# Performance work log

Measured on AMD Instinct MI355X. Metric: run time of the kernel, lower is better.

## Reference

```python
import jax, jax.numpy as jnp
import numpy as np

H = 64  # LSTM units for both layers
T = 128  # sequence length
D = 128  # input feature dim
B = 2048  # batch

def setup_inputs() -> dict:
    key = jax.random.key(0)
    ks = jax.random.split(key, 7)
    s_in = 1.0 / np.sqrt(D)
    s_h = 1.0 / np.sqrt(H)
    return {
        "x": jax.random.normal(ks[0], (B, T, D), dtype=jnp.float32),
        # Keras LSTM weights: kernel [in, 4H], recurrent_kernel [H, 4H], bias [4H]
        # gate order: i, f, g (cell candidate), o
        "W1": jax.random.normal(ks[1], (D, 4 * H), dtype=jnp.float32) * s_in,
        "U1": jax.random.normal(ks[2], (H, 4 * H), dtype=jnp.float32) * s_h,
        "b1": jnp.zeros((4 * H,), dtype=jnp.float32),
        "W2": jax.random.normal(ks[3], (H, 4 * H), dtype=jnp.float32) * s_h,
        "U2": jax.random.normal(ks[4], (H, 4 * H), dtype=jnp.float32) * s_h,
        "b2": jnp.zeros((4 * H,), dtype=jnp.float32),
    }

def _lstm(x, W, U, b, act):
    """Keras-faithful LSTM, return_sequences=True, zero init state.
    x: [B, T, D_in] -> hs: [B, T, H]
    recurrent_activation = sigmoid; `act` is the cell/output activation.
    """
    Bsz = x.shape[0]
    # Precompute input projections for all timesteps (one big GEMM).
    xz = jnp.einsum('btd,dg->btg', x, W) + b  # [B, T, 4H]
    xz = jnp.swapaxes(xz, 0, 1)  # [T, B, 4H]

    def step(carry, zt):
        h, c = carry
        z = zt + h @ U  # [B, 4H]
        i, f, g, o = jnp.split(z, 4, axis=-1)
        i = jax.nn.sigmoid(i)
        f = jax.nn.sigmoid(f)
        g = act(g)
        o = jax.nn.sigmoid(o)
        c = f * c + i * g
        h = o * act(c)
        return (h, c), h

    init = (jnp.zeros((Bsz, H), x.dtype), jnp.zeros((Bsz, H), x.dtype))
    _, hs = jax.lax.scan(step, init, xz)  # hs: [T, B, H]
    return jnp.swapaxes(hs, 0, 1)  # [B, T, H]

def reference(x, W1, U1, b1, W2, U2, b2):
    h1 = _lstm(x, W1, U1, b1, jnp.tanh)           # layer 1: default tanh
    h2 = _lstm(h1, W2, U2, b2, jax.nn.sigmoid)    # layer 2: activation='sigmoid'
    return h2.reshape(h2.shape[0], T * H, 1)      # Reshape((8192, 1))
```

## Files before the change

### kernel.cpp

```cpp
#include <hip/hip_runtime.h>
#include <stdint.h>

typedef __attribute__((ext_vector_type(8))) short short8;
typedef __attribute__((ext_vector_type(2))) short short2_t;
typedef __attribute__((ext_vector_type(4))) float floatx4;

#define TT 128
#define DD 128

#define BARRIER_LDS() asm volatile("s_waitcnt lgkmcnt(0)\n\ts_barrier" ::: "memory")

__device__ __forceinline__ short f2bf(float f) {
  union { float f; uint32_t u; } v; v.f = f;
  uint32_t u = v.u;
  u += 0x7fffu + ((u >> 16) & 1u);
  return (short)(u >> 16);
}

__device__ __forceinline__ float sigf(float x) {
  return __builtin_amdgcn_rcpf(1.f + __expf(-x));
}
__device__ __forceinline__ float tanhf_(float x) {
  return 2.f * __builtin_amdgcn_rcpf(1.f + __expf(-2.f * x)) - 1.f;
}

__global__ void wtrans_all(const float* __restrict__ W1, const float* __restrict__ U1,
                           const float* __restrict__ W2, const float* __restrict__ U2,
                           short* __restrict__ w1t, short* __restrict__ u1t,
                           short* __restrict__ w2t, short* __restrict__ u2t) {
  int n = blockIdx.x;
  int k = threadIdx.x;
  w1t[n * 128 + k] = f2bf(W1[k * 256 + n]);
  if (k < 64) {
    u1t[n * 64 + k] = f2bf(U1[k * 256 + n]);
    w2t[n * 64 + k] = f2bf(W2[k * 256 + n]);
    u2t[n * 64 + k] = f2bf(U2[k * 256 + n]);
  }
}

__global__ __launch_bounds__(256, 2) void lstm_fused(
    const float* __restrict__ x,
    const short* __restrict__ w1t, const short* __restrict__ u1t,
    const short* __restrict__ w2t, const short* __restrict__ u2t,
    const float* __restrict__ b1, const float* __restrict__ b2,
    float* __restrict__ out) {
  __shared__ short hb1[2][4 * 80];
  __shared__ short hb2[2][4 * 80];
  __shared__ short xbuf[2][4 * 144];

  const int tid = threadIdx.x;
  const int w = tid >> 6;
  const int lane = tid & 63;
  const int mrow = lane & 15;
  const int quad = lane >> 4;
  const int rowbase = blockIdx.x * 4;
  const int colw = w * 16 + mrow;
  const int br_a = mrow >> 2;

  short8 w1r[4][4], u1r[4][2], w2r[4][2], u2r[4][2];
#pragma unroll
  for (int g = 0; g < 4; ++g) {
    const int n = g * 4 + w;
#pragma unroll
    for (int s = 0; s < 4; ++s)
      w1r[g][s] = *(const short8*)(w1t + n * 2048 + mrow * 128 + quad * 8 + s * 32);
#pragma unroll
    for (int s = 0; s < 2; ++s) {
      u1r[g][s] = *(const short8*)(u1t + n * 1024 + mrow * 64 + quad * 8 + s * 32);
      w2r[g][s] = *(const short8*)(w2t + n * 1024 + mrow * 64 + quad * 8 + s * 32);
      u2r[g][s] = *(const short8*)(u2t + n * 1024 + mrow * 64 + quad * 8 + s * 32);
    }
  }
  float bias1[4], bias2[4];
#pragma unroll
  for (int g = 0; g < 4; ++g) {
    bias1[g] = b1[g * 64 + colw];
    bias2[g] = b2[g * 64 + colw];
  }

  const int xr = tid >> 6;
  const int xc = (tid & 63) * 2;
  const float* xload = x + (size_t)(rowbase + xr) * (TT * DD) + xc;

  {
    short* z = (short*)hb2;
    for (int i = tid; i < 2 * 4 * 80; i += 256) z[i] = 0;
    float a0 = xload[0], a1 = xload[1];
    *(short2_t*)&xbuf[1][xr * 144 + xc] = short2_t{f2bf(a0), f2bf(a1)};
  }
  BARRIER_LDS();
  short8 xf[4];
#pragma unroll
  for (int s = 0; s < 4; ++s)
    xf[s] = *(const short8*)&xbuf[1][br_a * 144 + (quad + 4 * s) * 8];
  float xr0 = xload[DD], xr1 = xload[DD + 1];

  short8 h1f[2], h2f[2];
#pragma unroll
  for (int s = 0; s < 2; ++s)
#pragma unroll
    for (int j = 0; j < 8; ++j) { h1f[s][j] = 0; h2f[s][j] = 0; }
  float c1 = 0.f, c2 = 0.f;

#pragma unroll 1
  for (int t = 0; t < TT; ++t) {
    const int p = t & 1;

    floatx4 acc[4];
#pragma unroll
    for (int g = 0; g < 4; ++g) acc[g] = floatx4{0.f, 0.f, 0.f, 0.f};
#pragma unroll
    for (int g = 0; g < 4; ++g) {
#pragma unroll
      for (int s = 0; s < 4; ++s)
        acc[g] = __builtin_amdgcn_mfma_f32_16x16x32_bf16(xf[s], w1r[g][s], acc[g], 0, 0, 0);
#pragma unroll
      for (int s = 0; s < 2; ++s)
        acc[g] = __builtin_amdgcn_mfma_f32_16x16x32_bf16(h1f[s], u1r[g][s], acc[g], 0, 0, 0);
    }

    *(short2_t*)&xbuf[p][xr * 144 + xc] = short2_t{f2bf(xr0), f2bf(xr1)};
    {
      int tn = (t + 2 < TT) ? t + 2 : TT - 1;
      xr0 = xload[(size_t)tn * DD];
      xr1 = xload[(size_t)tn * DD + 1];
    }

    {
      float ig = sigf(acc[0][0] + bias1[0]);
      float fg = sigf(acc[1][0] + bias1[1]);
      float gg = tanhf_(acc[2][0] + bias1[2]);
      float og = sigf(acc[3][0] + bias1[3]);
      float c = fg * c1 + ig * gg;
      c1 = c;
      float h = og * tanhf_(c);
      hb1[p][quad * 80 + colw] = f2bf(h);
    }

    BARRIER_LDS();

#pragma unroll
    for (int s = 0; s < 2; ++s) {
      h1f[s] = *(const short8*)&hb1[p][br_a * 80 + (quad + 4 * s) * 8];
      h2f[s] = *(const short8*)&hb2[1 - p][br_a * 80 + (quad + 4 * s) * 8];
    }
#pragma unroll
    for (int s = 0; s < 4; ++s)
      xf[s] = *(const short8*)&xbuf[p][br_a * 144 + (quad + 4 * s) * 8];

    floatx4 bcc[4];
#pragma unroll
    for (int g = 0; g < 4; ++g) bcc[g] = floatx4{0.f, 0.f, 0.f, 0.f};
#pragma unroll
    for (int g = 0; g < 4; ++g) {
#pragma unroll
      for (int s = 0; s < 2; ++s)
        bcc[g] = __builtin_amdgcn_mfma_f32_16x16x32_bf16(h1f[s], w2r[g][s], bcc[g], 0, 0, 0);
#pragma unroll
      for (int s = 0; s < 2; ++s)
        bcc[g] = __builtin_amdgcn_mfma_f32_16x16x32_bf16(h2f[s], u2r[g][s], bcc[g], 0, 0, 0);
    }

    {
      float ig = sigf(bcc[0][0] + bias2[0]);
      float fg = sigf(bcc[1][0] + bias2[1]);
      float gg = sigf(bcc[2][0] + bias2[2]);
      float og = sigf(bcc[3][0] + bias2[3]);
      float c = fg * c2 + ig * gg;
      c2 = c;
      float h = og * sigf(c);
      hb2[p][quad * 80 + colw] = f2bf(h);
      out[(size_t)(rowbase + quad) * 8192 + t * 64 + colw] = h;
    }
  }
}

extern "C" void kernel_launch(void* const* d_in, const int* in_sizes, int n_in,
                              void* d_out, int out_size, void* d_ws, size_t ws_size,
                              hipStream_t stream) {
  const float* x  = (const float*)d_in[0];
  const float* W1 = (const float*)d_in[1];
  const float* U1 = (const float*)d_in[2];
  const float* b1 = (const float*)d_in[3];
  const float* W2 = (const float*)d_in[4];
  const float* U2 = (const float*)d_in[5];
  const float* b2 = (const float*)d_in[6];
  float* out = (float*)d_out;

  short* w1t = (short*)d_ws;
  short* u1t = w1t + 32768;
  short* w2t = u1t + 16384;
  short* u2t = w2t + 16384;

  hipLaunchKernelGGL(wtrans_all, dim3(256), dim3(128), 0, stream,
                     W1, U1, W2, U2, w1t, u1t, w2t, u2t);
  hipLaunchKernelGGL(lstm_fused, dim3(512), dim3(256), 0, stream,
                     x, w1t, u1t, w2t, u2t, b1, b2, out);
}
```

Baseline: 316.7 us.

## Split LSTM layers across warp groups and pipeline layer 2 one step behind

Each block now processes 8 batch rows with 512 threads. Warps 0-3 run layer 1 while warps 4-7 run layer 2 one timestep behind, so the two layers execute concurrently with one barrier per step instead of running serially within the same warps. Each MFMA output tile now uses two of its four accumulator rows, which halves wasted MFMA work, and weights are split between the warp groups, lowering per-thread register pressure. The cost is an extra pipeline step, halved grid size (256 blocks), and layer-2 warps also taking over the x prefetch.

```diff
diff --git a/kernel.cpp b/kernel.cpp
--- a/kernel.cpp
+++ b/kernel.cpp
@@ -2,7 +2,7 @@
 #include <stdint.h>
 
 typedef __attribute__((ext_vector_type(8))) short short8;
-typedef __attribute__((ext_vector_type(2))) short short2_t;
+typedef __attribute__((ext_vector_type(4))) short short4_t;
 typedef __attribute__((ext_vector_type(4))) float floatx4;
 
 #define TT 128
@@ -38,139 +38,173 @@
   }
 }
 
-__global__ __launch_bounds__(256, 2) void lstm_fused(
+__global__ __launch_bounds__(512, 2) void lstm_fused(
     const float* __restrict__ x,
     const short* __restrict__ w1t, const short* __restrict__ u1t,
     const short* __restrict__ w2t, const short* __restrict__ u2t,
     const float* __restrict__ b1, const float* __restrict__ b2,
     float* __restrict__ out) {
-  __shared__ short hb1[2][4 * 80];
-  __shared__ short hb2[2][4 * 80];
-  __shared__ short xbuf[2][4 * 144];
+  __shared__ short hb1[2][8 * 80];
+  __shared__ short hb2[2][8 * 80];
+  __shared__ short xbuf[2][8 * 144];
 
   const int tid = threadIdx.x;
   const int w = tid >> 6;
+  const bool isL1 = (w < 4);
+  const int wg = w & 3;
   const int lane = tid & 63;
   const int mrow = lane & 15;
   const int quad = lane >> 4;
-  const int rowbase = blockIdx.x * 4;
-  const int colw = w * 16 + mrow;
-  const int br_a = mrow >> 2;
-
-  short8 w1r[4][4], u1r[4][2], w2r[4][2], u2r[4][2];
-#pragma unroll
-  for (int g = 0; g < 4; ++g) {
-    const int n = g * 4 + w;
+  const int rowbase = blockIdx.x * 8;
+  const int colw = wg * 16 + mrow;
+  const int br_a = 2 * (mrow >> 2) + (mrow & 1);
+
+  short8 wA[4][4], uA[4][2];
+  float bias[4];
+  if (isL1) {
+#pragma unroll
+    for (int g = 0; g < 4; ++g) {
+      const int n = g * 4 + wg;
+#pragma unroll
+      for (int s = 0; s < 4; ++s)
+        wA[g][s] = *(const short8*)(w1t + n * 2048 + mrow * 128 + quad * 8 + s * 32);
+#pragma unroll
+      for (int s = 0; s < 2; ++s)
+        uA[g][s] = *(const short8*)(u1t + n * 1024 + mrow * 64 + quad * 8 + s * 32);
+      bias[g] = b1[g * 64 + colw];
+    }
+  } else {
+#pragma unroll
+    for (int g = 0; g < 4; ++g) {
+      const int n = g * 4 + wg;
+#pragma unroll
+      for (int s = 0; s < 2; ++s) {
+        wA[g][s]     = *(const short8*)(w2t + n * 1024 + mrow * 64 + quad * 8 + s * 32);
+        wA[g][2 + s] = *(const short8*)(u2t + n * 1024 + mrow * 64 + quad * 8 + s * 32);
+      }
+      bias[g] = b2[g * 64 + colw];
+    }
+  }
+
+  const int tid2 = tid & 255;
+  const int sxr = tid2 >> 5;
+  const int sxc = (tid2 & 31) * 4;
+  const float* xload = x + (size_t)(rowbase + sxr) * (TT * DD) + sxc;
+
+  short8 h1f[2], xh[4];
+#pragma unroll
+  for (int s = 0; s < 2; ++s)
+#pragma unroll
+    for (int j = 0; j < 8; ++j) h1f[s][j] = 0;
+#pragma unroll
+  for (int s = 0; s < 4; ++s)
+#pragma unroll
+    for (int j = 0; j < 8; ++j) xh[s][j] = 0;
+  float cc[2] = {0.f, 0.f};
+  floatx4 xnext;
+
+  for (int idx = tid; idx < 2 * 8 * 80; idx += 512) ((short*)hb2)[idx] = 0;
+  if (!isL1) {
+    floatx4 x0 = *(const floatx4*)xload;
+    short4_t v;
+#pragma unroll
+    for (int j = 0; j < 4; ++j) v[j] = f2bf(x0[j]);
+    *(short4_t*)&xbuf[0][sxr * 144 + sxc] = v;
+    xnext = *(const floatx4*)(xload + DD);
+  }
+  BARRIER_LDS();
+  if (isL1) {
 #pragma unroll
     for (int s = 0; s < 4; ++s)
-      w1r[g][s] = *(const short8*)(w1t + n * 2048 + mrow * 128 + quad * 8 + s * 32);
-#pragma unroll
-    for (int s = 0; s < 2; ++s) {
-      u1r[g][s] = *(const short8*)(u1t + n * 1024 + mrow * 64 + quad * 8 + s * 32);
-      w2r[g][s] = *(const short8*)(w2t + n * 1024 + mrow * 64 + quad * 8 + s * 32);
-      u2r[g][s] = *(const short8*)(u2t + n * 1024 + mrow * 64 + quad * 8 + s * 32);
-    }
-  }
-  float bias1[4], bias2[4];
-#pragma unroll
-  for (int g = 0; g < 4; ++g) {
-    bias1[g] = b1[g * 64 + colw];
-    bias2[g] = b2[g * 64 + colw];
-  }
-
-  const int xr = tid >> 6;
-  const int xc = (tid & 63) * 2;
-  const float* xload = x + (size_t)(rowbase + xr) * (TT * DD) + xc;
-
-  {
-    short* z = (short*)hb2;
-    for (int i = tid; i < 2 * 4 * 80; i += 256) z[i] = 0;
-    float a0 = xload[0], a1 = xload[1];
-    *(short2_t*)&xbuf[1][xr * 144 + xc] = short2_t{f2bf(a0), f2bf(a1)};
-  }
-  BARRIER_LDS();
-  short8 xf[4];
-#pragma unroll
-  for (int s = 0; s < 4; ++s)
-    xf[s] = *(const short8*)&xbuf[1][br_a * 144 + (quad + 4 * s) * 8];
-  float xr0 = xload[DD], xr1 = xload[DD + 1];
-
-  short8 h1f[2], h2f[2];
-#pragma unroll
-  for (int s = 0; s < 2; ++s)
-#pragma unroll
-    for (int j = 0; j < 8; ++j) { h1f[s][j] = 0; h2f[s][j] = 0; }
-  float c1 = 0.f, c2 = 0.f;
+      xh[s] = *(const short8*)&xbuf[0][br_a * 144 + (quad + 4 * s) * 8];
+  }
+
+  float* outp = out + (size_t)rowbase * 8192 + colw;
 
 #pragma unroll 1
-  for (int t = 0; t < TT; ++t) {
-    const int p = t & 1;
-
-    floatx4 acc[4];
-#pragma unroll
-    for (int g = 0; g < 4; ++g) acc[g] = floatx4{0.f, 0.f, 0.f, 0.f};
-#pragma unroll
-    for (int g = 0; g < 4; ++g) {
-#pragma unroll
-      for (int s = 0; s < 4; ++s)
-        acc[g] = __builtin_amdgcn_mfma_f32_16x16x32_bf16(xf[s], w1r[g][s], acc[g], 0, 0, 0);
-#pragma unroll
-      for (int s = 0; s < 2; ++s)
-        acc[g] = __builtin_amdgcn_mfma_f32_16x16x32_bf16(h1f[s], u1r[g][s], acc[g], 0, 0, 0);
-    }
-
-    *(short2_t*)&xbuf[p][xr * 144 + xc] = short2_t{f2bf(xr0), f2bf(xr1)};
-    {
-      int tn = (t + 2 < TT) ? t + 2 : TT - 1;
-      xr0 = xload[(size_t)tn * DD];
-      xr1 = xload[(size_t)tn * DD + 1];
-    }
-
-    {
-      float ig = sigf(acc[0][0] + bias1[0]);
-      float fg = sigf(acc[1][0] + bias1[1]);
-      float gg = tanhf_(acc[2][0] + bias1[2]);
-      float og = sigf(acc[3][0] + bias1[3]);
-      float c = fg * c1 + ig * gg;
-      c1 = c;
-      float h = og * tanhf_(c);
-      hb1[p][quad * 80 + colw] = f2bf(h);
+  for (int i = 0; i <= TT; ++i) {
+    const int p = i & 1;
+
+    if (isL1) {
+      if (i < TT) {
+        floatx4 acc[4];
+#pragma unroll
+        for (int g = 0; g < 4; ++g) acc[g] = floatx4{0.f, 0.f, 0.f, 0.f};
+#pragma unroll
+        for (int g = 0; g < 4; ++g) {
+#pragma unroll
+          for (int s = 0; s < 4; ++s)
+            acc[g] = __builtin_amdgcn_mfma_f32_16x16x32_bf16(xh[s], wA[g][s], acc[g], 0, 0, 0);
+#pragma unroll
+          for (int s = 0; s < 2; ++s)
+            acc[g] = __builtin_amdgcn_mfma_f32_16x16x32_bf16(h1f[s], uA[g][s], acc[g], 0, 0, 0);
+        }
+#pragma unroll
+        for (int r = 0; r < 2; ++r) {
+          float ig = sigf(acc[0][r] + bias[0]);
+          float fg = sigf(acc[1][r] + bias[1]);
+          float gg = tanhf_(acc[2][r] + bias[2]);
+          float og = sigf(acc[3][r] + bias[3]);
+          float c = fg * cc[r] + ig * gg;
+          cc[r] = c;
+          float h = og * tanhf_(c);
+          hb1[p][(2 * quad + r) * 80 + colw] = f2bf(h);
+        }
+      }
+    } else {
+      {
+        short4_t v;
+#pragma unroll
+        for (int j = 0; j < 4; ++j) v[j] = f2bf(xnext[j]);
+        *(short4_t*)&xbuf[1 - p][sxr * 144 + sxc] = v;
+        int tn = (i + 2 < TT) ? i + 2 : TT - 1;
+        xnext = *(const floatx4*)(xload + (size_t)tn * DD);
+      }
+      if (i >= 1) {
+        floatx4 acc[4];
+#pragma unroll
+        for (int g = 0; g < 4; ++g) acc[g] = floatx4{0.f, 0.f, 0.f, 0.f};
+#pragma unroll
+        for (int g = 0; g < 4; ++g) {
+#pragma unroll
+          for (int s = 0; s < 2; ++s)
+            acc[g] = __builtin_amdgcn_mfma_f32_16x16x32_bf16(h1f[s], wA[g][s], acc[g], 0, 0, 0);
+#pragma unroll
+          for (int s = 0; s < 2; ++s)
+            acc[g] = __builtin_amdgcn_mfma_f32_16x16x32_bf16(xh[s], wA[g][2 + s], acc[g], 0, 0, 0);
+        }
+#pragma unroll
+        for (int r = 0; r < 2; ++r) {
+          float ig = sigf(acc[0][r] + bias[0]);
+          float fg = sigf(acc[1][r] + bias[1]);
+          float gg = sigf(acc[2][r] + bias[2]);
+          float og = sigf(acc[3][r] + bias[3]);
+          float c = fg * cc[r] + ig * gg;
+          cc[r] = c;
+          float h = og * sigf(c);
+          hb2[p][(2 * quad + r) * 80 + colw] = f2bf(h);
+          outp[(size_t)(2 * quad + r) * 8192 + (i - 1) * 64] = h;
+        }
+      }
     }
 
     BARRIER_LDS();
 
-#pragma unroll
-    for (int s = 0; s < 2; ++s) {
-      h1f[s] = *(const short8*)&hb1[p][br_a * 80 + (quad + 4 * s) * 8];
-      h2f[s] = *(const short8*)&hb2[1 - p][br_a * 80 + (quad + 4 * s) * 8];
-    }
-#pragma unroll
-    for (int s = 0; s < 4; ++s)
-      xf[s] = *(const short8*)&xbuf[p][br_a * 144 + (quad + 4 * s) * 8];
-
-    floatx4 bcc[4];
-#pragma unroll
-    for (int g = 0; g < 4; ++g) bcc[g] = floatx4{0.f, 0.f, 0.f, 0.f};
-#pragma unroll
-    for (int g = 0; g < 4; ++g) {
-#pragma unroll
-      for (int s = 0; s < 2; ++s)
-        bcc[g] = __builtin_amdgcn_mfma_f32_16x16x32_bf16(h1f[s], w2r[g][s], bcc[g], 0, 0, 0);
-#pragma unroll
-      for (int s = 0; s < 2; ++s)
-        bcc[g] = __builtin_amdgcn_mfma_f32_16x16x32_bf16(h2f[s], u2r[g][s], bcc[g], 0, 0, 0);
-    }
-
-    {
-      float ig = sigf(bcc[0][0] + bias2[0]);
-      float fg = sigf(bcc[1][0] + bias2[1]);
-      float gg = sigf(bcc[2][0] + bias2[2]);
-      float og = sigf(bcc[3][0] + bias2[3]);
-      float c = fg * c2 + ig * gg;
-      c2 = c;
-      float h = og * sigf(c);
-      hb2[p][quad * 80 + colw] = f2bf(h);
-      out[(size_t)(rowbase + quad) * 8192 + t * 64 + colw] = h;
+    if (i < TT) {
+      if (isL1) {
+#pragma unroll
+        for (int s = 0; s < 2; ++s)
+          h1f[s] = *(const short8*)&hb1[p][br_a * 80 + (quad + 4 * s) * 8];
+#pragma unroll
+        for (int s = 0; s < 4; ++s)
+          xh[s] = *(const short8*)&xbuf[1 - p][br_a * 144 + (quad + 4 * s) * 8];
+      } else {
+#pragma unroll
+        for (int s = 0; s < 2; ++s) {
+          h1f[s] = *(const short8*)&hb1[p][br_a * 80 + (quad + 4 * s) * 8];
+          xh[s]  = *(const short8*)&hb2[p][br_a * 80 + (quad + 4 * s) * 8];
+        }
+      }
     }
   }
 }
@@ -194,6 +228,6 @@
 
   hipLaunchKernelGGL(wtrans_all, dim3(256), dim3(128), 0, stream,
                      W1, U1, W2, U2, w1t, u1t, w2t, u2t);
-  hipLaunchKernelGGL(lstm_fused, dim3(512), dim3(256), 0, stream,
+  hipLaunchKernelGGL(lstm_fused, dim3(256), dim3(512), 0, stream,
                      x, w1t, u1t, w2t, u2t, b1, b2, out);
 }
```

Measured after the change: 286.0 us. -9.7%, faster.
